# Kernel tuning notes

Hardware: AMD Instinct MI355X
Metric: run time of the kernel (lower is better)

Reference implementation:

```python
import jax, jax.numpy as jnp
import numpy as np

# Config constants (match init_kwargs)
D_MODEL = 1024
D_MLP = 2048
NUM_EXPERTS = 8
EXPERTS_PER_TOKEN = 2
BATCH, SEQ = 2, 2048


def setup_inputs() -> dict:
    key = jax.random.key(0)
    k0, k1, k2, k3, k4 = jax.random.split(key, 5)
    init = lambda k, shape: jax.random.normal(k, shape, jnp.float32) * 0.02
    return {
        "x": jax.random.normal(k0, (BATCH, SEQ, D_MODEL), jnp.float32),
        "W_router": init(k1, (D_MODEL, NUM_EXPERTS)),
        "W_gate": init(k2, (NUM_EXPERTS, D_MODEL, D_MLP)),
        "W_in": init(k3, (NUM_EXPERTS, D_MODEL, D_MLP)),
        "W_out": init(k4, (NUM_EXPERTS, D_MLP, D_MODEL)),
    }


def reference(x, W_router, W_gate, W_in, W_out):
    B, S, D = x.shape
    h = x.reshape(-1, D)                                  # [T, D]
    T = h.shape[0]
    E = W_router.shape[1]

    # Router: softmax in fp32, top-k, renormalize (as in torch source)
    router_logits = h @ W_router                          # [T, E]
    probs = jax.nn.softmax(router_logits.astype(jnp.float32), axis=-1)
    top_w, top_i = jax.lax.top_k(probs, EXPERTS_PER_TOKEN)  # [T, K]
    top_w = top_w / top_w.sum(axis=-1, keepdims=True)
    top_w = top_w.astype(h.dtype)

    # Dense combine matrix [T, E]; top-k indices are distinct per token
    combine = jnp.zeros((T, E), h.dtype).at[jnp.arange(T)[:, None], top_i].set(top_w)

    # GatedMLP per expert: silu(h @ Wg) * (h @ Wi) @ Wo  (computed densely over experts,
    # then combined with the sparse routing weights -> same math as gather/MLP/scatter loop)
    gate_pre = jnp.einsum('td,edf->etf', h, W_gate)       # [E, T, F]
    up = jnp.einsum('td,edf->etf', h, W_in)               # [E, T, F]
    act = jax.nn.silu(gate_pre) * up                      # [E, T, F]
    expert_out = jnp.einsum('etf,efd->etd', act, W_out)   # [E, T, D]

    out = jnp.einsum('etd,te->td', expert_out, combine)   # [T, D]
    return out.reshape(B, S, D), router_logits
```

## Files before the change

### kernel.cpp

```cpp
#include <hip/hip_runtime.h>
#include <cstdint>
#include <cstddef>

#define T_TOK 4096
#define DM 1024
#define DF 2048
#define NE 8
#define PADROWS 9216
#define MAXTILES 72

typedef unsigned short u16;
typedef unsigned int u32;
using short8 = __attribute__((ext_vector_type(8))) short;
using f32x4  = __attribute__((ext_vector_type(4))) float;

static constexpr size_t OFF_H    = 0;
static constexpr size_t OFF_WGT  = OFF_H   + (size_t)T_TOK * DM * 2;
static constexpr size_t OFF_WIT  = OFF_WGT + (size_t)NE * DM * DF * 2;
static constexpr size_t OFF_WOT  = OFF_WIT + (size_t)NE * DM * DF * 2;
static constexpr size_t OFF_A    = OFF_WOT + (size_t)NE * DF * DM * 2;
static constexpr size_t OFF_TOK  = OFF_A   + (size_t)PADROWS * DF * 2;
static constexpr size_t OFF_WL   = OFF_TOK + PADROWS * 4;
static constexpr size_t OFF_TEXP = OFF_WL  + PADROWS * 4;
static constexpr size_t OFF_TW   = OFF_TEXP + (size_t)T_TOK * 2 * 4;
static constexpr size_t OFF_CNT  = OFF_TW  + (size_t)T_TOK * 2 * 4;
static constexpr size_t OFF_CUR  = OFF_CNT + 64;
static constexpr size_t OFF_NT   = OFF_CUR + 64;
static constexpr size_t OFF_TE   = OFF_NT  + 64;
static constexpr size_t OFF_TP   = OFF_TE  + 512;
static constexpr size_t OFF_ZPG  = OFF_TP  + 512;
static constexpr size_t OFF_POS  = OFF_ZPG + 4096;

__device__ __forceinline__ u16 f2bf(float f) {
  u32 u = __builtin_bit_cast(u32, f);
  u += 0x7FFFu + ((u >> 16) & 1u);
  return (u16)(u >> 16);
}

__device__ __forceinline__ void async16(const void* g, void* l) {
  __builtin_amdgcn_global_load_lds((__attribute__((address_space(1))) void*)(g),
                                   (__attribute__((address_space(3))) void*)(l),
                                   16, 0, 0);
}

__global__ void convert_x_k(const float4* __restrict__ x, u16* __restrict__ h) {
  size_t i = (size_t)blockIdx.x * 256 + threadIdx.x;
  float4 v = x[i];
  u32 lo = (u32)f2bf(v.x) | ((u32)f2bf(v.y) << 16);
  u32 hi = (u32)f2bf(v.z) | ((u32)f2bf(v.w) << 16);
  uint2 o; o.x = lo; o.y = hi;
  *(uint2*)&h[i * 4] = o;
}

__global__ void init_small_k(int* __restrict__ tok, float* __restrict__ wl,
                             int* __restrict__ cnt, u16* __restrict__ zpg) {
  int i = blockIdx.x * 256 + threadIdx.x;
  if (i < PADROWS) { tok[i] = -1; wl[i] = 0.f; }
  if (i < NE) cnt[i] = 0;
  if (i < 2048) zpg[i] = 0;
}

__global__ void transpose_w_k(const float* __restrict__ Wg, const float* __restrict__ Wi,
                              const float* __restrict__ Wo, u16* __restrict__ wgT,
                              u16* __restrict__ wiT, u16* __restrict__ woT) {
  __shared__ u16 lT[64][65];
  int bid = blockIdx.x;
  int mat = bid >> 12;
  int r = bid & 4095;
  const float* src; u16* dst; int R, C;
  if (mat == 0)      { src = Wg; dst = wgT; R = DM; C = DF; }
  else if (mat == 1) { src = Wi; dst = wiT; R = DM; C = DF; }
  else               { src = Wo; dst = woT; R = DF; C = DM; }
  int e = r >> 9;
  int rem = r & 511;
  int ctiles = C >> 6;
  int tr = rem / ctiles, tc = rem % ctiles;
  size_t eb = (size_t)e * R * C;
  int r0 = tr * 64, c0 = tc * 64;
  int wv = threadIdx.x >> 6, lane = threadIdx.x & 63;
#pragma unroll
  for (int it = 0; it < 16; ++it) {
    int rl = it * 4 + wv;
    float v = src[eb + (size_t)(r0 + rl) * C + c0 + lane];
    lT[lane][rl] = f2bf(v);
  }
  __syncthreads();
#pragma unroll
  for (int it = 0; it < 16; ++it) {
    int cl = it * 4 + wv;
    dst[eb + (size_t)(c0 + cl) * R + r0 + lane] = lT[cl][lane];
  }
}

__global__ void router_k(const float* __restrict__ x, const float* __restrict__ Wr,
                         float* __restrict__ logits, int* __restrict__ texp,
                         float* __restrict__ tw, int* __restrict__ cnt) {
  int wv = threadIdx.x >> 6, lane = threadIdx.x & 63;
  int t = blockIdx.x * 4 + wv;
  const float* h = x + (size_t)t * DM;
  float acc[8] = {0.f, 0.f, 0.f, 0.f, 0.f, 0.f, 0.f, 0.f};
#pragma unroll
  for (int j = 0; j < 16; ++j) {
    float hv = h[lane + j * 64];
    const float4* wr = (const float4*)(Wr + (size_t)(lane + j * 64) * 8);
    float4 w0 = wr[0], w1 = wr[1];
    acc[0] += hv * w0.x; acc[1] += hv * w0.y; acc[2] += hv * w0.z; acc[3] += hv * w0.w;
    acc[4] += hv * w1.x; acc[5] += hv * w1.y; acc[6] += hv * w1.z; acc[7] += hv * w1.w;
  }
#pragma unroll
  for (int e = 0; e < 8; ++e)
#pragma unroll
    for (int off = 32; off > 0; off >>= 1) acc[e] += __shfl_down(acc[e], off, 64);
  if (lane == 0) {
    float mx = acc[0];
#pragma unroll
    for (int e = 1; e < 8; ++e) mx = fmaxf(mx, acc[e]);
    float p[8];
#pragma unroll
    for (int e = 0; e < 8; ++e) p[e] = __expf(acc[e] - mx);
    int i1 = 0; float b1 = p[0];
#pragma unroll
    for (int e = 1; e < 8; ++e) if (p[e] > b1) { b1 = p[e]; i1 = e; }
    int i2 = -1; float b2 = -1.f;
#pragma unroll
    for (int e = 0; e < 8; ++e) if (e != i1 && p[e] > b2) { b2 = p[e]; i2 = e; }
    float inv = 1.f / (b1 + b2);
    texp[t * 2] = i1; texp[t * 2 + 1] = i2;
    tw[t * 2] = b1 * inv; tw[t * 2 + 1] = b2 * inv;
    atomicAdd(&cnt[i1], 1); atomicAdd(&cnt[i2], 1);
#pragma unroll
    for (int e = 0; e < 8; ++e) logits[(size_t)t * 8 + e] = acc[e];
  }
}

__global__ void plan_k(const int* __restrict__ cnt, int* __restrict__ cursor,
                       int* __restrict__ tile_e, int* __restrict__ tile_p,
                       int* __restrict__ ntiles) {
  if (threadIdx.x == 0) {
    int off = 0, nt = 0;
    for (int e = 0; e < NE; ++e) {
      cursor[e] = off;
      int n = cnt[e];
      int t = (n + 127) >> 7;
      for (int i = 0; i < t; ++i) { tile_e[nt] = e; tile_p[nt] = off + i * 128; ++nt; }
      off += t * 128;
    }
    *ntiles = nt;
  }
}

__global__ void scatter_k(const int* __restrict__ texp, const float* __restrict__ tw,
                          int* __restrict__ cursor, int* __restrict__ tok,
                          float* __restrict__ wl, int* __restrict__ pos) {
  int t = blockIdx.x * 256 + threadIdx.x;
#pragma unroll
  for (int k = 0; k < 2; ++k) {
    int e = texp[t * 2 + k];
    int p = atomicAdd(&cursor[e], 1);
    tok[p] = t;
    wl[p] = tw[t * 2 + k];
    pos[t * 2 + k] = p;
  }
}

__global__ __launch_bounds__(256) void gemm1_k(
    const u16* __restrict__ hbf, const u16* __restrict__ wgT, const u16* __restrict__ wiT,
    const int* __restrict__ tok, const float* __restrict__ wl,
    const int* __restrict__ tile_e, const int* __restrict__ tile_p,
    const int* __restrict__ ntiles, const u16* __restrict__ zpg,
    u16* __restrict__ Aact) {
  __shared__ char smem[65536];
  const int tile = blockIdx.y;
  if (tile >= *ntiles) return;
  const int e  = tile_e[tile];
  const int p0 = tile_p[tile];
  const int f0 = blockIdx.x * 64;
  const int tid = threadIdx.x, wv = tid >> 6, lane = tid & 63;

  const u16* hsrc[4];
  int hoff[4];
#pragma unroll
  for (int i = 0; i < 4; ++i) {
    const int row = wv * 32 + i * 8 + (lane >> 3);
    const int gc  = (lane & 7) ^ (row & 7);
    const int tk  = tok[p0 + row];
    hsrc[i] = (tk >= 0) ? (hbf + (size_t)tk * DM + gc * 8) : (zpg + gc * 8);
    hoff[i] = (wv * 32 + i * 8) * 64;
  }
  const u16* wbase = ((wv < 2) ? wgT : wiT) + (size_t)e * DM * DF;
  const int half = wv & 1, mt = wv >> 1;
  const u16* bsrc[4];
  int boff[4];
#pragma unroll
  for (int i = 0; i < 4; ++i) {
    const int row = half * 32 + i * 8 + (lane >> 3);
    const int gc  = (lane & 7) ^ (row & 7);
    bsrc[i] = wbase + (size_t)(f0 + row) * DM + gc * 8;
    boff[i] = 8192 + mt * 4096 + (half * 32 + i * 8) * 64;
  }

  f32x4 accG[4][2], accU[4][2];
#pragma unroll
  for (int m = 0; m < 4; ++m)
#pragma unroll
    for (int n = 0; n < 2; ++n) { accG[m][n] = (f32x4)(0.f); accU[m][n] = (f32x4)(0.f); }

  const int wr = wv >> 1, wc = wv & 1;
  const int wrBase = wr * 64, wcBase = wc * 32;
  const int l4 = lane >> 4, ln = lane & 15;

  {
    u16* b = (u16*)smem;
#pragma unroll
    for (int i = 0; i < 4; ++i) async16(hsrc[i], b + hoff[i]);
#pragma unroll
    for (int i = 0; i < 4; ++i) async16(bsrc[i], b + boff[i]);
  }
  __syncthreads();

  int cur = 0;
  for (int kt = 0; kt < DM / 64; ++kt) {
    if (kt < DM / 64 - 1) {
      u16* b = (u16*)smem + (cur ^ 1) * 16384;
#pragma unroll
      for (int i = 0; i < 4; ++i) async16(hsrc[i] + (size_t)(kt + 1) * 64, b + hoff[i]);
#pragma unroll
      for (int i = 0; i < 4; ++i) async16(bsrc[i] + (size_t)(kt + 1) * 64, b + boff[i]);
    }
    const u16* b = (const u16*)smem + cur * 16384;
#pragma unroll
    for (int s = 0; s < 2; ++s) {
      const int c = s * 4 + l4;
      short8 a[4], bg[2], bu[2];
#pragma unroll
      for (int m = 0; m < 4; ++m) {
        const int row = wrBase + m * 16 + ln;
        a[m] = *(const short8*)&b[row * 64 + ((c ^ (row & 7)) * 8)];
      }
#pragma unroll
      for (int n = 0; n < 2; ++n) {
        const int rowb = wcBase + n * 16 + ln;
        const int so = rowb * 64 + ((c ^ (rowb & 7)) * 8);
        bg[n] = *(const short8*)&b[8192 + so];
        bu[n] = *(const short8*)&b[12288 + so];
      }
#pragma unroll
      for (int m = 0; m < 4; ++m)
#pragma unroll
        for (int n = 0; n < 2; ++n) {
          accG[m][n] = __builtin_amdgcn_mfma_f32_16x16x32_bf16(a[m], bg[n], accG[m][n], 0, 0, 0);
          accU[m][n] = __builtin_amdgcn_mfma_f32_16x16x32_bf16(a[m], bu[n], accU[m][n], 0, 0, 0);
        }
    }
    __syncthreads();
    cur ^= 1;
  }

  u16* lOut = (u16*)smem;
#pragma unroll
  for (int m = 0; m < 4; ++m)
#pragma unroll
    for (int j = 0; j < 4; ++j) {
      const int row = wrBase + m * 16 + l4 * 4 + j;
      const float w = wl[p0 + row];
#pragma unroll
      for (int n = 0; n < 2; ++n) {
        const float g = accG[m][n][j];
        const float u = accU[m][n][j];
        const float val = (g / (1.f + __expf(-g))) * u * w;
        lOut[row * 80 + wcBase + n * 16 + ln] = f2bf(val);
      }
    }
  __syncthreads();
  const int r = tid >> 1, hf = tid & 1;
  u16* gdst = Aact + (size_t)(p0 + r) * DF + f0 + hf * 32;
  const u16* lsrc = &lOut[r * 80 + hf * 32];
#pragma unroll
  for (int i = 0; i < 4; ++i)
    *(short8*)(gdst + i * 8) = *(const short8*)(lsrc + i * 8);
}

__global__ __launch_bounds__(256) void gemm2_k(
    const u16* __restrict__ Aact, const u16* __restrict__ woT,
    const int* __restrict__ tile_e, const int* __restrict__ tile_p,
    const int* __restrict__ ntiles, float* __restrict__ scr) {
  __shared__ char smem[65536];
  const int tile = blockIdx.y;
  if (tile >= *ntiles) return;
  const int e  = tile_e[tile];
  const int p0 = tile_p[tile];
  const int d0 = blockIdx.x * 128;
  const int tid = threadIdx.x, wv = tid >> 6, lane = tid & 63;

  const u16* asrc[4];
  int aoff[4];
#pragma unroll
  for (int i = 0; i < 4; ++i) {
    const int row = wv * 32 + i * 8 + (lane >> 3);
    const int gc  = (lane & 7) ^ (row & 7);
    asrc[i] = Aact + (size_t)(p0 + row) * DF + gc * 8;
    aoff[i] = (wv * 32 + i * 8) * 64;
  }
  const u16* wb = woT + (size_t)e * DM * DF;
  const u16* wsrc[4];
  int woff[4];
#pragma unroll
  for (int i = 0; i < 4; ++i) {
    const int row = wv * 32 + i * 8 + (lane >> 3);
    const int gc  = (lane & 7) ^ (row & 7);
    wsrc[i] = wb + (size_t)(d0 + row) * DF + gc * 8;
    woff[i] = 8192 + (wv * 32 + i * 8) * 64;
  }

  f32x4 acc[4][4];
#pragma unroll
  for (int m = 0; m < 4; ++m)
#pragma unroll
    for (int n = 0; n < 4; ++n) acc[m][n] = (f32x4)(0.f);

  const int wr = wv >> 1, wc = wv & 1;
  const int wrBase = wr * 64, wcBase = wc * 64;
  const int l4 = lane >> 4, ln = lane & 15;

  {
    u16* b = (u16*)smem;
#pragma unroll
    for (int i = 0; i < 4; ++i) async16(asrc[i], b + aoff[i]);
#pragma unroll
    for (int i = 0; i < 4; ++i) async16(wsrc[i], b + woff[i]);
  }
  __syncthreads();

  int cur = 0;
  for (int kt = 0; kt < DF / 64; ++kt) {
    if (kt < DF / 64 - 1) {
      u16* b = (u16*)smem + (cur ^ 1) * 16384;
#pragma unroll
      for (int i = 0; i < 4; ++i) async16(asrc[i] + (size_t)(kt + 1) * 64, b + aoff[i]);
#pragma unroll
      for (int i = 0; i < 4; ++i) async16(wsrc[i] + (size_t)(kt + 1) * 64, b + woff[i]);
    }
    const u16* b = (const u16*)smem + cur * 16384;
#pragma unroll
    for (int s = 0; s < 2; ++s) {
      const int c = s * 4 + l4;
      short8 a[4], bw[4];
#pragma unroll
      for (int m = 0; m < 4; ++m) {
        const int row = wrBase + m * 16 + ln;
        a[m] = *(const short8*)&b[row * 64 + ((c ^ (row & 7)) * 8)];
      }
#pragma unroll
      for (int n = 0; n < 4; ++n) {
        const int rowb = wcBase + n * 16 + ln;
        bw[n] = *(const short8*)&b[8192 + rowb * 64 + ((c ^ (rowb & 7)) * 8)];
      }
#pragma unroll
      for (int m = 0; m < 4; ++m)
#pragma unroll
        for (int n = 0; n < 4; ++n)
          acc[m][n] = __builtin_amdgcn_mfma_f32_16x16x32_bf16(a[m], bw[n], acc[m][n], 0, 0, 0);
    }
    __syncthreads();
    cur ^= 1;
  }

#pragma unroll
  for (int m = 0; m < 4; ++m)
#pragma unroll
    for (int j = 0; j < 4; ++j) {
      const int row = wrBase + m * 16 + l4 * 4 + j;
      float* dst = scr + (size_t)(p0 + row) * DM + d0;
#pragma unroll
      for (int n = 0; n < 4; ++n)
        dst[wcBase + n * 16 + ln] = acc[m][n][j];
    }
}

__global__ void combine_k(const float* __restrict__ scr, const int* __restrict__ pos,
                          float* __restrict__ out) {
  const int t = blockIdx.x;
  const int d = threadIdx.x;
  const int p1 = pos[t * 2], p2 = pos[t * 2 + 1];
  const float4 a = *(const float4*)(scr + (size_t)p1 * DM + d * 4);
  const float4 b = *(const float4*)(scr + (size_t)p2 * DM + d * 4);
  float4 o;
  o.x = a.x + b.x; o.y = a.y + b.y; o.z = a.z + b.z; o.w = a.w + b.w;
  *(float4*)(out + (size_t)t * DM + d * 4) = o;
}

extern "C" void kernel_launch(void* const* d_in, const int* in_sizes, int n_in,
                              void* d_out, int out_size, void* d_ws, size_t ws_size,
                              hipStream_t stream) {
  const float* x  = (const float*)d_in[0];
  const float* Wr = (const float*)d_in[1];
  const float* Wg = (const float*)d_in[2];
  const float* Wi = (const float*)d_in[3];
  const float* Wo = (const float*)d_in[4];
  float* outF = (float*)d_out;
  float* logits = outF + (size_t)T_TOK * DM;

  char* ws = (char*)d_ws;
  u16*  hbf   = (u16*)(ws + OFF_H);
  u16*  wgT   = (u16*)(ws + OFF_WGT);
  u16*  wiT   = (u16*)(ws + OFF_WIT);
  u16*  woT   = (u16*)(ws + OFF_WOT);
  u16*  Aact  = (u16*)(ws + OFF_A);
  int*  tok   = (int*)(ws + OFF_TOK);
  float* wl   = (float*)(ws + OFF_WL);
  int*  texp  = (int*)(ws + OFF_TEXP);
  float* tw   = (float*)(ws + OFF_TW);
  int*  cnt   = (int*)(ws + OFF_CNT);
  int*  cur   = (int*)(ws + OFF_CUR);
  int*  nt    = (int*)(ws + OFF_NT);
  int*  te    = (int*)(ws + OFF_TE);
  int*  tp    = (int*)(ws + OFF_TP);
  u16*  zpg   = (u16*)(ws + OFF_ZPG);
  int*  pos   = (int*)(ws + OFF_POS);
  float* scr  = (float*)(ws + OFF_WGT);

  convert_x_k<<<4096, 256, 0, stream>>>((const float4*)x, hbf);
  init_small_k<<<40, 256, 0, stream>>>(tok, wl, cnt, zpg);
  transpose_w_k<<<12288, 256, 0, stream>>>(Wg, Wi, Wo, wgT, wiT, woT);
  router_k<<<1024, 256, 0, stream>>>(x, Wr, logits, texp, tw, cnt);
  plan_k<<<1, 64, 0, stream>>>(cnt, cur, te, tp, nt);
  scatter_k<<<16, 256, 0, stream>>>(texp, tw, cur, tok, wl, pos);
  gemm1_k<<<dim3(DF / 64, MAXTILES), 256, 0, stream>>>(hbf, wgT, wiT, tok, wl, te, tp, nt, zpg, Aact);
  gemm2_k<<<dim3(DM / 128, MAXTILES), 256, 0, stream>>>(Aact, woT, te, tp, nt, scr);
  combine_k<<<4096, 256, 0, stream>>>(scr, pos, outF);
}
```

Baseline: 360.3 us.

## Deepen GEMM pipelines to four-stage BK=32 ring and store expert outputs as bf16

Both grouped GEMMs move from a double-buffered BK=64 loop with __syncthreads to a four-slot BK=32 ring that prefetches two stages ahead. Synchronisation uses explicit vmcnt waits and raw barriers, and s_setprio raises wave priority around the MFMA blocks. A new row-pair swizzled LDS layout replaces the old one, and padded token rows now load token 0 instead of a zero page. gemm2 stages its output through LDS and writes bf16 instead of fp32 partials, which halves scratch traffic into combine_k at the cost of rounding the per-expert outputs to bf16 before the sum.

```diff
diff --git a/kernel.cpp b/kernel.cpp
--- a/kernel.cpp
+++ b/kernel.cpp
@@ -28,19 +28,30 @@
 static constexpr size_t OFF_NT   = OFF_CUR + 64;
 static constexpr size_t OFF_TE   = OFF_NT  + 64;
 static constexpr size_t OFF_TP   = OFF_TE  + 512;
-static constexpr size_t OFF_ZPG  = OFF_TP  + 512;
-static constexpr size_t OFF_POS  = OFF_ZPG + 4096;
+static constexpr size_t OFF_POS  = OFF_TP  + 512;
 
 __device__ __forceinline__ u16 f2bf(float f) {
   u32 u = __builtin_bit_cast(u32, f);
   u += 0x7FFFu + ((u >> 16) & 1u);
   return (u16)(u >> 16);
 }
+__device__ __forceinline__ float bf2f(u16 b) {
+  u32 u = ((u32)b) << 16;
+  return __builtin_bit_cast(float, u);
+}
 
 __device__ __forceinline__ void async16(const void* g, void* l) {
   __builtin_amdgcn_global_load_lds((__attribute__((address_space(1))) void*)(g),
                                    (__attribute__((address_space(3))) void*)(l),
                                    16, 0, 0);
+}
+
+#define VM4() asm volatile("s_waitcnt vmcnt(4)" ::: "memory")
+#define VM0() asm volatile("s_waitcnt vmcnt(0)" ::: "memory")
+#define BAR() do { asm volatile("" ::: "memory"); __builtin_amdgcn_s_barrier(); asm volatile("" ::: "memory"); } while (0)
+
+__device__ __forceinline__ int lds_off(int row, int ko) {
+  return (row >> 1) * 64 + ((((row & 1) * 4 + ko) ^ ((row >> 1) & 7)) * 8);
 }
 
 __global__ void convert_x_k(const float4* __restrict__ x, u16* __restrict__ h) {
@@ -53,11 +64,10 @@
 }
 
 __global__ void init_small_k(int* __restrict__ tok, float* __restrict__ wl,
-                             int* __restrict__ cnt, u16* __restrict__ zpg) {
+                             int* __restrict__ cnt) {
   int i = blockIdx.x * 256 + threadIdx.x;
   if (i < PADROWS) { tok[i] = -1; wl[i] = 0.f; }
   if (i < NE) cnt[i] = 0;
-  if (i < 2048) zpg[i] = 0;
 }
 
 __global__ void transpose_w_k(const float* __restrict__ Wg, const float* __restrict__ Wi,
@@ -167,96 +177,90 @@
     const u16* __restrict__ hbf, const u16* __restrict__ wgT, const u16* __restrict__ wiT,
     const int* __restrict__ tok, const float* __restrict__ wl,
     const int* __restrict__ tile_e, const int* __restrict__ tile_p,
-    const int* __restrict__ ntiles, const u16* __restrict__ zpg,
-    u16* __restrict__ Aact) {
-  __shared__ char smem[65536];
+    const int* __restrict__ ntiles, u16* __restrict__ Aact) {
+  __shared__ u16 smem[32768];
   const int tile = blockIdx.y;
   if (tile >= *ntiles) return;
   const int e  = tile_e[tile];
   const int p0 = tile_p[tile];
   const int f0 = blockIdx.x * 64;
   const int tid = threadIdx.x, wv = tid >> 6, lane = tid & 63;
-
-  const u16* hsrc[4];
-  int hoff[4];
-#pragma unroll
-  for (int i = 0; i < 4; ++i) {
-    const int row = wv * 32 + i * 8 + (lane >> 3);
-    const int gc  = (lane & 7) ^ (row & 7);
-    const int tk  = tok[p0 + row];
-    hsrc[i] = (tk >= 0) ? (hbf + (size_t)tk * DM + gc * 8) : (zpg + gc * 8);
-    hoff[i] = (wv * 32 + i * 8) * 64;
-  }
-  const u16* wbase = ((wv < 2) ? wgT : wiT) + (size_t)e * DM * DF;
-  const int half = wv & 1, mt = wv >> 1;
-  const u16* bsrc[4];
-  int boff[4];
-#pragma unroll
-  for (int i = 0; i < 4; ++i) {
-    const int row = half * 32 + i * 8 + (lane >> 3);
-    const int gc  = (lane & 7) ^ (row & 7);
-    bsrc[i] = wbase + (size_t)(f0 + row) * DM + gc * 8;
-    boff[i] = 8192 + mt * 4096 + (half * 32 + i * 8) * 64;
-  }
-
-  f32x4 accG[4][2], accU[4][2];
-#pragma unroll
-  for (int m = 0; m < 4; ++m)
-#pragma unroll
-    for (int n = 0; n < 2; ++n) { accG[m][n] = (f32x4)(0.f); accU[m][n] = (f32x4)(0.f); }
+  const int ch = lane & 7, l8 = lane >> 3;
+
+  const u16* asrcp[2];
+#pragma unroll
+  for (int i = 0; i < 2; ++i) {
+    const int rp = (wv * 2 + i) * 8 + l8;
+    const int cc = ch ^ (rp & 7);
+    const int row = rp * 2 + (cc >> 2);
+    const int ko = cc & 3;
+    int tk = tok[p0 + row];
+    if (tk < 0) tk = 0;
+    asrcp[i] = hbf + (size_t)tk * DM + ko * 8;
+  }
+  const u16* bgsrc; const u16* busrc;
+  {
+    const int rp = wv * 8 + l8;
+    const int cc = ch ^ (rp & 7);
+    const int row = rp * 2 + (cc >> 2);
+    const int ko = cc & 3;
+    bgsrc = wgT + (size_t)e * DM * DF + (size_t)(f0 + row) * DM + ko * 8;
+    busrc = wiT + (size_t)e * DM * DF + (size_t)(f0 + row) * DM + ko * 8;
+  }
 
   const int wr = wv >> 1, wc = wv & 1;
   const int wrBase = wr * 64, wcBase = wc * 32;
   const int l4 = lane >> 4, ln = lane & 15;
-
-  {
-    u16* b = (u16*)smem;
-#pragma unroll
-    for (int i = 0; i < 4; ++i) async16(hsrc[i], b + hoff[i]);
-#pragma unroll
-    for (int i = 0; i < 4; ++i) async16(bsrc[i], b + boff[i]);
-  }
-  __syncthreads();
-
-  int cur = 0;
-  for (int kt = 0; kt < DM / 64; ++kt) {
-    if (kt < DM / 64 - 1) {
-      u16* b = (u16*)smem + (cur ^ 1) * 16384;
-#pragma unroll
-      for (int i = 0; i < 4; ++i) async16(hsrc[i] + (size_t)(kt + 1) * 64, b + hoff[i]);
-#pragma unroll
-      for (int i = 0; i < 4; ++i) async16(bsrc[i] + (size_t)(kt + 1) * 64, b + boff[i]);
+  int aoff[4], boff[2];
+#pragma unroll
+  for (int m = 0; m < 4; ++m) aoff[m] = lds_off(wrBase + m * 16 + ln, l4);
+#pragma unroll
+  for (int n = 0; n < 2; ++n) boff[n] = lds_off(wcBase + n * 16 + ln, l4);
+
+  f32x4 accG[4][2], accU[4][2];
+#pragma unroll
+  for (int m = 0; m < 4; ++m)
+#pragma unroll
+    for (int n = 0; n < 2; ++n) { accG[m][n] = (f32x4)(0.f); accU[m][n] = (f32x4)(0.f); }
+
+  auto STAGE = [&](int tt) {
+    u16* dst = smem + (tt & 3) * 8192;
+    const size_t kadd = (size_t)tt * 32;
+#pragma unroll
+    for (int i = 0; i < 2; ++i) async16(asrcp[i] + kadd, dst + (wv * 2 + i) * 512);
+    async16(bgsrc + kadd, dst + 4096 + wv * 512);
+    async16(busrc + kadd, dst + 6144 + wv * 512);
+  };
+
+  constexpr int NT = DM / 32;
+  STAGE(0); STAGE(1);
+  VM4(); BAR();
+
+  for (int t = 0; t < NT; ++t) {
+    const u16* b = smem + (t & 3) * 8192;
+    if (t + 2 < NT) STAGE(t + 2);
+    short8 af[4], bgf[2], buf_[2];
+#pragma unroll
+    for (int n = 0; n < 2; ++n) {
+      bgf[n]  = *(const short8*)&b[4096 + boff[n]];
+      buf_[n] = *(const short8*)&b[6144 + boff[n]];
     }
-    const u16* b = (const u16*)smem + cur * 16384;
-#pragma unroll
-    for (int s = 0; s < 2; ++s) {
-      const int c = s * 4 + l4;
-      short8 a[4], bg[2], bu[2];
-#pragma unroll
-      for (int m = 0; m < 4; ++m) {
-        const int row = wrBase + m * 16 + ln;
-        a[m] = *(const short8*)&b[row * 64 + ((c ^ (row & 7)) * 8)];
+#pragma unroll
+    for (int m = 0; m < 4; ++m) af[m] = *(const short8*)&b[aoff[m]];
+    __builtin_amdgcn_s_setprio(1);
+#pragma unroll
+    for (int m = 0; m < 4; ++m)
+#pragma unroll
+      for (int n = 0; n < 2; ++n) {
+        accG[m][n] = __builtin_amdgcn_mfma_f32_16x16x32_bf16(af[m], bgf[n], accG[m][n], 0, 0, 0);
+        accU[m][n] = __builtin_amdgcn_mfma_f32_16x16x32_bf16(af[m], buf_[n], accU[m][n], 0, 0, 0);
       }
-#pragma unroll
-      for (int n = 0; n < 2; ++n) {
-        const int rowb = wcBase + n * 16 + ln;
-        const int so = rowb * 64 + ((c ^ (rowb & 7)) * 8);
-        bg[n] = *(const short8*)&b[8192 + so];
-        bu[n] = *(const short8*)&b[12288 + so];
-      }
-#pragma unroll
-      for (int m = 0; m < 4; ++m)
-#pragma unroll
-        for (int n = 0; n < 2; ++n) {
-          accG[m][n] = __builtin_amdgcn_mfma_f32_16x16x32_bf16(a[m], bg[n], accG[m][n], 0, 0, 0);
-          accU[m][n] = __builtin_amdgcn_mfma_f32_16x16x32_bf16(a[m], bu[n], accU[m][n], 0, 0, 0);
-        }
-    }
-    __syncthreads();
-    cur ^= 1;
-  }
-
-  u16* lOut = (u16*)smem;
+    __builtin_amdgcn_s_setprio(0);
+    if (t + 2 < NT) { VM4(); } else if (t + 1 < NT) { VM0(); }
+    BAR();
+  }
+
+  u16* lOut = smem;
 #pragma unroll
   for (int m = 0; m < 4; ++m)
 #pragma unroll
@@ -283,109 +287,106 @@
 __global__ __launch_bounds__(256) void gemm2_k(
     const u16* __restrict__ Aact, const u16* __restrict__ woT,
     const int* __restrict__ tile_e, const int* __restrict__ tile_p,
-    const int* __restrict__ ntiles, float* __restrict__ scr) {
-  __shared__ char smem[65536];
+    const int* __restrict__ ntiles, u16* __restrict__ scr) {
+  __shared__ u16 smem[32768];
   const int tile = blockIdx.y;
   if (tile >= *ntiles) return;
   const int e  = tile_e[tile];
   const int p0 = tile_p[tile];
   const int d0 = blockIdx.x * 128;
   const int tid = threadIdx.x, wv = tid >> 6, lane = tid & 63;
-
-  const u16* asrc[4];
-  int aoff[4];
-#pragma unroll
-  for (int i = 0; i < 4; ++i) {
-    const int row = wv * 32 + i * 8 + (lane >> 3);
-    const int gc  = (lane & 7) ^ (row & 7);
-    asrc[i] = Aact + (size_t)(p0 + row) * DF + gc * 8;
-    aoff[i] = (wv * 32 + i * 8) * 64;
-  }
-  const u16* wb = woT + (size_t)e * DM * DF;
-  const u16* wsrc[4];
-  int woff[4];
-#pragma unroll
-  for (int i = 0; i < 4; ++i) {
-    const int row = wv * 32 + i * 8 + (lane >> 3);
-    const int gc  = (lane & 7) ^ (row & 7);
-    wsrc[i] = wb + (size_t)(d0 + row) * DF + gc * 8;
-    woff[i] = 8192 + (wv * 32 + i * 8) * 64;
-  }
-
-  f32x4 acc[4][4];
-#pragma unroll
-  for (int m = 0; m < 4; ++m)
-#pragma unroll
-    for (int n = 0; n < 4; ++n) acc[m][n] = (f32x4)(0.f);
+  const int ch = lane & 7, l8 = lane >> 3;
+
+  const u16* asrcp[2];
+  const u16* wsrcp[2];
+#pragma unroll
+  for (int i = 0; i < 2; ++i) {
+    const int rp = (wv * 2 + i) * 8 + l8;
+    const int cc = ch ^ (rp & 7);
+    const int row = rp * 2 + (cc >> 2);
+    const int ko = cc & 3;
+    asrcp[i] = Aact + (size_t)(p0 + row) * DF + ko * 8;
+    wsrcp[i] = woT + (size_t)e * DM * DF + (size_t)(d0 + row) * DF + ko * 8;
+  }
 
   const int wr = wv >> 1, wc = wv & 1;
   const int wrBase = wr * 64, wcBase = wc * 64;
   const int l4 = lane >> 4, ln = lane & 15;
-
-  {
-    u16* b = (u16*)smem;
-#pragma unroll
-    for (int i = 0; i < 4; ++i) async16(asrc[i], b + aoff[i]);
-#pragma unroll
-    for (int i = 0; i < 4; ++i) async16(wsrc[i], b + woff[i]);
-  }
-  __syncthreads();
-
-  int cur = 0;
-  for (int kt = 0; kt < DF / 64; ++kt) {
-    if (kt < DF / 64 - 1) {
-      u16* b = (u16*)smem + (cur ^ 1) * 16384;
-#pragma unroll
-      for (int i = 0; i < 4; ++i) async16(asrc[i] + (size_t)(kt + 1) * 64, b + aoff[i]);
-#pragma unroll
-      for (int i = 0; i < 4; ++i) async16(wsrc[i] + (size_t)(kt + 1) * 64, b + woff[i]);
-    }
-    const u16* b = (const u16*)smem + cur * 16384;
-#pragma unroll
-    for (int s = 0; s < 2; ++s) {
-      const int c = s * 4 + l4;
-      short8 a[4], bw[4];
-#pragma unroll
-      for (int m = 0; m < 4; ++m) {
-        const int row = wrBase + m * 16 + ln;
-        a[m] = *(const short8*)&b[row * 64 + ((c ^ (row & 7)) * 8)];
-      }
-#pragma unroll
-      for (int n = 0; n < 4; ++n) {
-        const int rowb = wcBase + n * 16 + ln;
-        bw[n] = *(const short8*)&b[8192 + rowb * 64 + ((c ^ (rowb & 7)) * 8)];
-      }
-#pragma unroll
-      for (int m = 0; m < 4; ++m)
-#pragma unroll
-        for (int n = 0; n < 4; ++n)
-          acc[m][n] = __builtin_amdgcn_mfma_f32_16x16x32_bf16(a[m], bw[n], acc[m][n], 0, 0, 0);
-    }
-    __syncthreads();
-    cur ^= 1;
-  }
-
+  int aoff[4], boff[4];
+#pragma unroll
+  for (int m = 0; m < 4; ++m) aoff[m] = lds_off(wrBase + m * 16 + ln, l4);
+#pragma unroll
+  for (int n = 0; n < 4; ++n) boff[n] = lds_off(wcBase + n * 16 + ln, l4);
+
+  f32x4 acc[4][4];
+#pragma unroll
+  for (int m = 0; m < 4; ++m)
+#pragma unroll
+    for (int n = 0; n < 4; ++n) acc[m][n] = (f32x4)(0.f);
+
+  auto STAGE = [&](int tt) {
+    u16* dst = smem + (tt & 3) * 8192;
+    const size_t kadd = (size_t)tt * 32;
+#pragma unroll
+    for (int i = 0; i < 2; ++i) async16(asrcp[i] + kadd, dst + (wv * 2 + i) * 512);
+#pragma unroll
+    for (int i = 0; i < 2; ++i) async16(wsrcp[i] + kadd, dst + 4096 + (wv * 2 + i) * 512);
+  };
+
+  constexpr int NT = DF / 32;
+  STAGE(0); STAGE(1);
+  VM4(); BAR();
+
+  for (int t = 0; t < NT; ++t) {
+    const u16* b = smem + (t & 3) * 8192;
+    if (t + 2 < NT) STAGE(t + 2);
+    short8 af[4], bw[4];
+#pragma unroll
+    for (int n = 0; n < 4; ++n) bw[n] = *(const short8*)&b[4096 + boff[n]];
+#pragma unroll
+    for (int m = 0; m < 4; ++m) af[m] = *(const short8*)&b[aoff[m]];
+    __builtin_amdgcn_s_setprio(1);
+#pragma unroll
+    for (int m = 0; m < 4; ++m)
+#pragma unroll
+      for (int n = 0; n < 4; ++n)
+        acc[m][n] = __builtin_amdgcn_mfma_f32_16x16x32_bf16(af[m], bw[n], acc[m][n], 0, 0, 0);
+    __builtin_amdgcn_s_setprio(0);
+    if (t + 2 < NT) { VM4(); } else if (t + 1 < NT) { VM0(); }
+    BAR();
+  }
+
+  u16* lOut = smem;
 #pragma unroll
   for (int m = 0; m < 4; ++m)
 #pragma unroll
     for (int j = 0; j < 4; ++j) {
       const int row = wrBase + m * 16 + l4 * 4 + j;
-      float* dst = scr + (size_t)(p0 + row) * DM + d0;
 #pragma unroll
       for (int n = 0; n < 4; ++n)
-        dst[wcBase + n * 16 + ln] = acc[m][n][j];
+        lOut[row * 136 + wcBase + n * 16 + ln] = f2bf(acc[m][n][j]);
     }
-}
-
-__global__ void combine_k(const float* __restrict__ scr, const int* __restrict__ pos,
+  __syncthreads();
+  const int r = tid >> 1, hf = tid & 1;
+  u16* gdst = scr + (size_t)(p0 + r) * DM + d0 + hf * 64;
+  const u16* lsrc = &lOut[r * 136 + hf * 64];
+#pragma unroll
+  for (int i = 0; i < 8; ++i)
+    *(short8*)(gdst + i * 8) = *(const short8*)(lsrc + i * 8);
+}
+
+__global__ void combine_k(const u16* __restrict__ scr, const int* __restrict__ pos,
                           float* __restrict__ out) {
   const int t = blockIdx.x;
   const int d = threadIdx.x;
   const int p1 = pos[t * 2], p2 = pos[t * 2 + 1];
-  const float4 a = *(const float4*)(scr + (size_t)p1 * DM + d * 4);
-  const float4 b = *(const float4*)(scr + (size_t)p2 * DM + d * 4);
+  const ushort4 a = *(const ushort4*)(scr + (size_t)p1 * DM + d * 4);
+  const ushort4 b = *(const ushort4*)(scr + (size_t)p2 * DM + d * 4);
   float4 o;
-  o.x = a.x + b.x; o.y = a.y + b.y; o.z = a.z + b.z; o.w = a.w + b.w;
+  o.x = bf2f(a.x) + bf2f(b.x);
+  o.y = bf2f(a.y) + bf2f(b.y);
+  o.z = bf2f(a.z) + bf2f(b.z);
+  o.w = bf2f(a.w) + bf2f(b.w);
   *(float4*)(out + (size_t)t * DM + d * 4) = o;
 }
 
@@ -415,17 +416,16 @@
   int*  nt    = (int*)(ws + OFF_NT);
   int*  te    = (int*)(ws + OFF_TE);
   int*  tp    = (int*)(ws + OFF_TP);
-  u16*  zpg   = (u16*)(ws + OFF_ZPG);
   int*  pos   = (int*)(ws + OFF_POS);
-  float* scr  = (float*)(ws + OFF_WGT);
+  u16*  scr   = (u16*)(ws + OFF_WGT);
 
   convert_x_k<<<4096, 256, 0, stream>>>((const float4*)x, hbf);
-  init_small_k<<<40, 256, 0, stream>>>(tok, wl, cnt, zpg);
+  init_small_k<<<40, 256, 0, stream>>>(tok, wl, cnt);
   transpose_w_k<<<12288, 256, 0, stream>>>(Wg, Wi, Wo, wgT, wiT, woT);
   router_k<<<1024, 256, 0, stream>>>(x, Wr, logits, texp, tw, cnt);
   plan_k<<<1, 64, 0, stream>>>(cnt, cur, te, tp, nt);
   scatter_k<<<16, 256, 0, stream>>>(texp, tw, cur, tok, wl, pos);
-  gemm1_k<<<dim3(DF / 64, MAXTILES), 256, 0, stream>>>(hbf, wgT, wiT, tok, wl, te, tp, nt, zpg, Aact);
+  gemm1_k<<<dim3(DF / 64, MAXTILES), 256, 0, stream>>>(hbf, wgT, wiT, tok, wl, te, tp, nt, Aact);
   gemm2_k<<<dim3(DM / 128, MAXTILES), 256, 0, stream>>>(Aact, woT, te, tp, nt, scr);
   combine_k<<<4096, 256, 0, stream>>>(scr, pos, outF);
 }
```

New measurement: 377.6 us. 1.05x slower.
